# Optimization experiments

Measured on AMD Instinct MI355X. Metric: run time of the kernel, lower is better.

## Reference

```python
import jax, jax.numpy as jnp
import numpy as np

LEAK = 0.01  # PyTorch LeakyReLU default negative_slope


def _leaky(x):
    return jnp.where(x >= 0, x, LEAK * x)


def _sim1(x, ws):
    # 7-layer 1x1-conv MLP applied per pixel; x: (..., Cin, H, W)
    n = len(ws)
    for i, w in enumerate(ws):
        x = jnp.einsum('oc,...chw->...ohw', w, x)
        if i < n - 1:
            x = _leaky(x)
    return x


def setup_inputs() -> dict:
    key = jax.random.key(0)
    ks = jax.random.split(key, 9)
    B, C, S, K = 8, 256, 15, 17
    d = {
        'template_feature': jax.random.normal(ks[0], (B, C, S, S), jnp.float32),
        'candidate_feature': jax.random.normal(ks[1], (B, C, S + K - 1, S + K - 1), jnp.float32),
    }
    chans = [(C, 2 * C), (C // 2, C), (C // 4, C // 2), (C // 8, C // 4),
             (C // 16, C // 8), (C // 32, C // 16), (1, C // 32)]
    for i, (o, c) in enumerate(chans):
        # kaiming_normal_ fan_out for a 1x1 conv: std = sqrt(2/out_channels)
        d[f'w{i}'] = jax.random.normal(ks[2 + i], (o, c), jnp.float32) * np.sqrt(2.0 / o).astype(np.float32)
    return d


def reference(template_feature, candidate_feature, w0, w1, w2, w3, w4, w5, w6):
    ws = (w0, w1, w2, w3, w4, w5, w6)
    B, C, S, _ = template_feature.shape
    K = 17  # sliding-window grid (31-15+1)

    # ---- template branch ----
    t_mean = jnp.mean(template_feature, axis=(-2, -1), keepdims=True)
    rep = jnp.concatenate([jnp.broadcast_to(t_mean, template_feature.shape),
                           template_feature], axis=1)  # (B, 2C, S, S)
    w = _sim1(rep, ws)  # (B, 1, S, S)
    wn = jax.nn.softmax(w.reshape(B, 1, -1), axis=2).reshape(B, 1, S, S)
    common_template = jnp.sum(template_feature * wn, axis=(-2, -1)).reshape(B, C, 1, 1)

    # ---- candidate branch: im2col of 15x15 windows over 31x31 -> 17x17 grid ----
    ii = jnp.arange(S)[:, None] + jnp.arange(K)[None, :]  # (S, K): in-window + window-offset
    # cand_all[b,c,i,j,p,q] = candidate[b,c, i+p, j+q]  -> (B, C, S, S, K, K)
    cand_all = candidate_feature[:, :, ii[:, None, :, None], ii[None, :, None, :]]
    c_mean = jnp.mean(cand_all, axis=(2, 3), keepdims=True)  # divide by S*S as in original
    rep_c = jnp.concatenate([jnp.broadcast_to(c_mean, cand_all.shape), cand_all], axis=1)  # (B, 2C, S, S, K, K)
    rep_c = jnp.transpose(rep_c, (0, 4, 5, 1, 2, 3))  # (B, K, K, 2C, S, S)
    w_c = _sim1(rep_c, ws)  # (B, K, K, 1, S, S)
    wcn = jax.nn.softmax(w_c.reshape(B, K, K, 1, -1), axis=-1).reshape(B, K, K, 1, S, S)
    wcn = jnp.transpose(wcn, (0, 3, 4, 5, 1, 2))  # (B, 1, S, S, K, K)
    common_candidate = jnp.sum(cand_all * wcn, axis=(2, 3))  # (B, C, K, K)

    return common_template, common_candidate
```

## Files before the change

### kernel.cpp

```cpp
#include <hip/hip_runtime.h>

typedef _Float16 half_t;
typedef half_t half4 __attribute__((ext_vector_type(4)));
typedef half_t half8 __attribute__((ext_vector_type(8)));
typedef __fp16 pk16x2 __attribute__((ext_vector_type(2)));
typedef float  f32x4 __attribute__((ext_vector_type(4)));
typedef float  f32x2 __attribute__((ext_vector_type(2)));

static __device__ __forceinline__ half4 pack4(f32x4 a) {
  pk16x2 lo = __builtin_amdgcn_cvt_pkrtz(a[0], a[1]);
  pk16x2 hi = __builtin_amdgcn_cvt_pkrtz(a[2], a[3]);
  half4 h;
  h[0] = lo[0]; h[1] = lo[1]; h[2] = hi[0]; h[3] = hi[1];
  return h;
}

constexpr int B_  = 8;
constexpr int S_  = 15;
constexpr int K_  = 17;
constexpr int P_  = 31;
constexpr int SS_ = 225;
constexpr int PP_ = 961;
constexpr int KK_ = 289;

constexpr int NROW_C = B_ * PP_;
constexpr int NROW_T = B_ * SS_;
constexpr int NROW   = NROW_C + NROW_T;

constexpr int NW0H = 512 * 256;
constexpr int NF16 = 128*256 + 64*128 + 32*64;

constexpr size_t OFF_IN   = 0;
constexpr size_t OFF_OUT0 = OFF_IN   + (size_t)NROW * 256;
constexpr size_t OFF_ROWS = OFF_OUT0 + (size_t)NROW * 512;
constexpr size_t OFF_M0   = OFF_ROWS + (size_t)B_ * 31 * 17 * 256;
constexpr size_t OFF_TM0  = OFF_M0   + (size_t)B_ * KK_ * 256;
constexpr size_t OFF_F16  = OFF_TM0  + (size_t)B_ * 256;

constexpr int X0B  = 0;
constexpr int X1B  = 16384;
constexpr int X3TB = 16384;
constexpr int Y4B  = 25600;
constexpr int SMB  = 32768;
constexpr int REDB = 33728;
constexpr int W4B  = 33792;
constexpr int W5B  = 36096;
constexpr int W6B  = 36736;
constexpr int ROWB = 36768;
constexpr int LDSB = 37248;

__global__ __launch_bounds__(256) void prep_kernel(
    const float* __restrict__ templ, const float* __restrict__ cand,
    const float* __restrict__ w0, const float* __restrict__ w1,
    const float* __restrict__ w2, const float* __restrict__ w3,
    float* __restrict__ inarr, half_t* __restrict__ w0h,
    half_t* __restrict__ w1h, half_t* __restrict__ w2h,
    half_t* __restrict__ w3h)
{
  const int NA = NROW_C * 256;
  const int NB = NROW_T * 256;
  const int total = NA + NB + NW0H + NF16;
  for (int idx = blockIdx.x * blockDim.x + threadIdx.x; idx < total;
       idx += gridDim.x * blockDim.x) {
    if (idx < NA) {
      int c = idx & 255; int r = idx >> 8;
      int q = r % P_; int p = (r / P_) % P_; int b = r / PP_;
      inarr[idx] = cand[((b * 256 + c) * P_ + p) * P_ + q];
    } else if (idx < NA + NB) {
      int t = idx - NA;
      int c = t & 255; int r = t >> 8;
      int j = r % S_; int i = (r / S_) % S_; int b = r / SS_;
      inarr[idx] = templ[((b * 256 + c) * S_ + i) * S_ + j];
    } else if (idx < NA + NB + NW0H) {
      int t = idx - NA - NB;
      int m = t >> 8; int c = t & 255;
      w0h[t] = (half_t)(m < 256 ? w0[m * 512 + 256 + c] : w0[(m - 256) * 512 + c]);
    } else {
      int t = idx - NA - NB - NW0H;
      if (t < 32768)      w1h[t] = (half_t)w1[t];
      else if (t < 40960) w2h[t - 32768] = (half_t)w2[t - 32768];
      else                w3h[t - 40960] = (half_t)w3[t - 40960];
    }
  }
}

__global__ __launch_bounds__(512) void l0gemm_kernel(
    const float* __restrict__ in, const half_t* __restrict__ w0h,
    float* __restrict__ out0)
{
  __shared__ __align__(16) char xls[16 * 512];
  const int tid  = threadIdx.x;
  const int lane = tid & 63;
  const int wvs  = tid >> 6;
  const int row0 = blockIdx.x * 16;

  {
    const int row = tid >> 5;
    const int c8  = (tid & 31) * 8;
    const float* src = in + (size_t)(row0 + row) * 256 + c8;
    half8 h;
#pragma unroll
    for (int r = 0; r < 8; ++r) h[r] = (half_t)src[r];
    const int off = (row * 512 + c8 * 2) ^ ((row & 7) << 4);
    *(half8*)(xls + off) = h;
  }
  __syncthreads();

  const int l15 = lane & 15, g = lane >> 4;
  f32x4 acc[4];
#pragma unroll
  for (int mt = 0; mt < 4; ++mt) acc[mt] = (f32x4){0.f, 0.f, 0.f, 0.f};
#pragma unroll 2
  for (int kb = 0; kb < 8; ++kb) {
    const int off = (l15 * 512 + kb * 64 + g * 16) ^ ((l15 & 7) << 4);
    half8 bfr = *(const half8*)(xls + off);
#pragma unroll
    for (int mt = 0; mt < 4; ++mt) {
      const half_t* ap = w0h + (size_t)((wvs * 4 + mt) * 16 + l15) * 256 + kb * 32 + g * 8;
      half8 a = *(const half8*)ap;
      acc[mt] = __builtin_amdgcn_mfma_f32_16x16x32_f16(a, bfr, acc[mt], 0, 0, 0);
    }
  }
#pragma unroll
  for (int mt = 0; mt < 4; ++mt) {
    const int m0c = (wvs * 4 + mt) * 16 + g * 4;
    *(f32x4*)(out0 + (size_t)(row0 + l15) * 512 + m0c) = acc[mt];
  }
}

__global__ __launch_bounds__(256) void rowsum_kernel(
    const float* __restrict__ out0, float* __restrict__ rows)
{
  const int bid = blockIdx.x;
  const int o = threadIdx.x;
  const int v = bid % 17; const int p = (bid / 17) % 31; const int b = bid / (17 * 31);
  float s = 0.f;
  for (int j = 0; j < 15; ++j)
    s += out0[(size_t)(b * PP_ + p * P_ + v + j) * 512 + 256 + o];
  rows[(size_t)bid * 256 + o] = s;
}

__global__ __launch_bounds__(256) void colsum_kernel(
    const float* __restrict__ rows, float* __restrict__ m0v)
{
  const int bid = blockIdx.x;
  const int o = threadIdx.x;
  const int v = bid % 17; const int u = (bid / 17) % 17; const int b = bid / KK_;
  float s = 0.f;
  for (int i = 0; i < 15; ++i)
    s += rows[(size_t)((b * 31 + u + i) * 17 + v) * 256 + o];
  m0v[(size_t)bid * 256 + o] = s * (1.0f / 225.0f);
}

__global__ __launch_bounds__(256) void tmean0_kernel(
    const float* __restrict__ out0, float* __restrict__ tm0v)
{
  const int b = blockIdx.x;
  const int o = threadIdx.x;
  float s = 0.f;
  for (int t = 0; t < SS_; ++t)
    s += out0[(size_t)(NROW_C + b * SS_ + t) * 512 + 256 + o];
  tm0v[b * 256 + o] = s * (1.0f / 225.0f);
}

__global__ __launch_bounds__(512, 4) void chain_kernel(
    const float* __restrict__ out0, const float* __restrict__ m0v,
    const float* __restrict__ tm0v,
    const half_t* __restrict__ w1h, const half_t* __restrict__ w2h,
    const half_t* __restrict__ w3h,
    const float* __restrict__ w4, const float* __restrict__ w5,
    const float* __restrict__ w6,
    const float* __restrict__ inarr, float* __restrict__ out)
{
  __shared__ __align__(16) char lds[LDSB];
  float*    ldsf   = (float*)lds;
  float*    sm     = (float*)(lds + SMB);
  float*    red    = (float*)(lds + REDB);
  uint16_t* rowoff = (uint16_t*)(lds + ROWB);

  const int tid  = threadIdx.x;
  const int lane = tid & 63;
  const int wvs  = __builtin_amdgcn_readfirstlane(tid >> 6);
  const int bid  = (blockIdx.x & 7) * 290 + (blockIdx.x >> 3);
  const bool is_t = (bid >= B_ * KK_);
  int b, u = 0, v = 0;
  const float* mean_vec;
  if (!is_t) {
    b = bid / KK_;
    int r = bid % KK_;
    u = r / K_; v = r % K_;
    mean_vec = m0v + (size_t)bid * 256;
  } else {
    b = bid - B_ * KK_;
    mean_vec = tm0v + (size_t)b * 256;
  }

  if (tid < SS_) {
    int i = tid / 15, j = tid - i * 15;
    rowoff[tid] = is_t ? (uint16_t)(NROW_C + b * SS_ + tid)
                       : (uint16_t)(b * PP_ + (u + i) * P_ + (v + j));
  }
  ((float*)(lds + W4B))[(tid >> 5) * 36 + (tid & 31)] = w4[tid];
  if (tid < 128) ((float*)(lds + W5B))[(tid >> 4) * 20 + (tid & 15)] = w5[tid];
  if (tid < 8)   ((float*)(lds + W6B))[tid] = w6[tid];

  const half_t* w1base = w1h + (size_t)(16 * wvs + (lane & 15)) * 256 + ((lane >> 4) << 3);
  const int g2 = wvs & 3, h2 = wvs >> 2;
  half8 af2[4];
  {
    const half_t* base = w2h + (size_t)(16 * g2 + (lane & 15)) * 128 + ((lane >> 4) << 3);
#pragma unroll
    for (int kb = 0; kb < 4; ++kb) af2[kb] = *(const half8*)(base + kb * 32);
  }
  const int rt3 = wvs & 1, ct3 = wvs >> 1;
  const half_t* b3ptr = w3h + (size_t)(16 * rt3 + (lane & 15)) * 64 + ((lane >> 4) << 3);
  const int l31 = lane & 31, lhi = lane >> 5;
  const f32x4 mv4a = *(const f32x4*)(mean_vec + 4 * l31);
  const f32x4 mv4b = *(const f32x4*)(mean_vec + 128 + 4 * l31);
  __syncthreads();

  for (int ti = 0; ti < 4; ++ti) {
    const int s0 = ti * 64;
    const int cnt = min(64, SS_ - s0);

    f32x4 acc[4];
#pragma unroll
    for (int nt = 0; nt < 4; ++nt) acc[nt] = (f32x4){0.f, 0.f, 0.f, 0.f};
#pragma unroll
    for (int h = 0; h < 2; ++h) {
      const f32x4 mvh = h ? mv4b : mv4a;
      for (int tt = 0; tt < 4; ++tt) {
        const int pos = 2 * (wvs + tt * 8) + lhi;
        const int srow = rowoff[min(s0 + pos, SS_ - 1)];
        f32x4 x = *(const f32x4*)(out0 + ((size_t)srow << 9) + h * 128 + 4 * l31);
        f32x4 a;
#pragma unroll
        for (int r = 0; r < 4; ++r) {
          float t2 = x[r] + mvh[r];
          a[r] = fmaxf(t2, 0.01f * t2);
        }
        const int off = (pos * 256 + l31 * 8) ^ ((pos & 7) << 4);
        *(half4*)(lds + X0B + off) = pack4(a);
      }
      __syncthreads();

      {
        const half_t* w1p = w1base;
        asm volatile("" : "+v"(w1p));
#pragma unroll 2
        for (int kbp = 0; kbp < 4; ++kbp) {
          half8 a1 = *(const half8*)(w1p + (h * 4 + kbp) * 32);
          const int kbyte = kbp * 64 + ((lane >> 4) << 4);
#pragma unroll
          for (int nt = 0; nt < 4; ++nt) {
            const int pos = nt * 16 + (lane & 15);
            const int off = (pos * 256 + kbyte) ^ ((pos & 7) << 4);
            half8 bfr = *(const half8*)(lds + X0B + off);
            acc[nt] = __builtin_amdgcn_mfma_f32_16x16x32_f16(a1, bfr, acc[nt], 0, 0, 0);
          }
        }
      }
      if (h == 1) {
#pragma unroll
        for (int nt = 0; nt < 4; ++nt) {
          const int pos = nt * 16 + (lane & 15);
          f32x4 a;
#pragma unroll
          for (int r = 0; r < 4; ++r) a[r] = fmaxf(acc[nt][r], 0.01f * acc[nt][r]);
          const int ch0 = 16 * wvs + ((lane >> 4) << 2);
          const int off = (pos * 256 + ch0 * 2) ^ ((pos & 7) << 4);
          *(half4*)(lds + X1B + off) = pack4(a);
        }
      }
      __syncthreads();
    }

    f32x4 acc2[2];
#pragma unroll
    for (int nt = 0; nt < 2; ++nt) acc2[nt] = (f32x4){0.f, 0.f, 0.f, 0.f};
#pragma unroll
    for (int kb = 0; kb < 4; ++kb) {
      const int kbyte = kb * 64 + ((lane >> 4) << 4);
#pragma unroll
      for (int nt = 0; nt < 2; ++nt) {
        const int pos = h2 * 32 + nt * 16 + (lane & 15);
        const int off = (pos * 256 + kbyte) ^ ((pos & 7) << 4);
        half8 bfr = *(const half8*)(lds + X1B + off);
        acc2[nt] = __builtin_amdgcn_mfma_f32_16x16x32_f16(af2[kb], bfr, acc2[nt], 0, 0, 0);
      }
    }
#pragma unroll
    for (int nt = 0; nt < 2; ++nt) {
      const int pos = h2 * 32 + nt * 16 + (lane & 15);
      const int ch0 = 16 * g2 + ((lane >> 4) << 2);
      f32x4 a;
#pragma unroll
      for (int r = 0; r < 4; ++r) a[r] = fmaxf(acc2[nt][r], 0.01f * acc2[nt][r]);
      const int off = (pos * 128 + ch0 * 2) ^ ((pos & 7) << 4);
      *(half4*)(lds + X0B + off) = pack4(a);
    }
    __syncthreads();

    {
      f32x4 acc3 = (f32x4){0.f, 0.f, 0.f, 0.f};
      const int pos = ct3 * 16 + (lane & 15);
#pragma unroll
      for (int kb = 0; kb < 2; ++kb) {
        half8 a3 = *(const half8*)(b3ptr + kb * 32);
        const int kbyte = kb * 64 + ((lane >> 4) << 4);
        const int off = (pos * 128 + kbyte) ^ ((pos & 7) << 4);
        half8 bfr = *(const half8*)(lds + X0B + off);
        acc3 = __builtin_amdgcn_mfma_f32_16x16x32_f16(a3, bfr, acc3, 0, 0, 0);
      }
      const int ch0 = 16 * rt3 + ((lane >> 4) << 2);
      f32x4 o4;
#pragma unroll
      for (int r = 0; r < 4; ++r) o4[r] = fmaxf(acc3[r], 0.01f * acc3[r]);
      *(f32x4*)(lds + X3TB + pos * 144 + ch0 * 4) = o4;
    }
    __syncthreads();

    {
      const int p = lane >> 3, g = lane & 7;
      const int pos = 8 * wvs + p;
      float a4_0 = 0.f, a4_1 = 0.f;
#pragma unroll
      for (int c0 = 0; c0 < 32; c0 += 4) {
        f32x4 x  = *(const f32x4*)(lds + X3TB + pos * 144 + c0 * 4);
        f32x4 wA = *(const f32x4*)(lds + W4B + (2 * g) * 144 + c0 * 4);
        f32x4 wB = *(const f32x4*)(lds + W4B + (2 * g + 1) * 144 + c0 * 4);
#pragma unroll
        for (int r = 0; r < 4; ++r) {
          a4_0 = fmaf(wA[r], x[r], a4_0);
          a4_1 = fmaf(wB[r], x[r], a4_1);
        }
      }
      f32x2 y4v;
      y4v[0] = fmaxf(a4_0, 0.01f * a4_0);
      y4v[1] = fmaxf(a4_1, 0.01f * a4_1);
      *(f32x2*)(lds + Y4B + pos * 80 + g * 8) = y4v;
      float a5 = 0.f;
#pragma unroll
      for (int c0 = 0; c0 < 16; c0 += 4) {
        f32x4 x = *(const f32x4*)(lds + Y4B + pos * 80 + c0 * 4);
        f32x4 w = *(const f32x4*)(lds + W5B + g * 80 + c0 * 4);
#pragma unroll
        for (int r = 0; r < 4; ++r) a5 = fmaf(w[r], x[r], a5);
      }
      a5 = fmaxf(a5, 0.01f * a5);
      float t6 = ((float*)(lds + W6B))[g] * a5;
      t6 += __shfl_xor(t6, 1);
      t6 += __shfl_xor(t6, 2);
      t6 += __shfl_xor(t6, 4);
      if (g == 0 && (8 * wvs + p) < cnt) sm[s0 + pos] = t6;
    }
    __syncthreads();
  }

  float vv = (tid < SS_) ? sm[tid] : -1e30f;
  float m = vv;
#pragma unroll
  for (int off = 32; off >= 1; off >>= 1) m = fmaxf(m, __shfl_xor(m, off));
  if (lane == 0) red[wvs] = m;
  __syncthreads();
  m = red[0];
#pragma unroll
  for (int w = 1; w < 8; ++w) m = fmaxf(m, red[w]);
  float e = (tid < SS_) ? __expf(vv - m) : 0.f;
  float ss = e;
#pragma unroll
  for (int off = 32; off >= 1; off >>= 1) ss += __shfl_xor(ss, off);
  __syncthreads();
  if (lane == 0) red[wvs] = ss;
  __syncthreads();
  float Stot = red[0];
#pragma unroll
  for (int w = 1; w < 8; ++w) Stot += red[w];
  if (tid < SS_) sm[tid] = e / Stot;
  __syncthreads();

  {
    const int c2 = (tid & 127) * 2;
    const int q  = tid >> 7;
    float accx = 0.f, accy = 0.f;
    for (int s = q; s < SS_; s += 4) {
      f32x2 ft = *(const f32x2*)(inarr + ((size_t)rowoff[s] << 8) + c2);
      float w = sm[s];
      accx = fmaf(w, ft[0], accx);
      accy = fmaf(w, ft[1], accy);
    }
    __syncthreads();
    ldsf[q * 256 + c2]     = accx;
    ldsf[q * 256 + c2 + 1] = accy;
    __syncthreads();
    if (tid < 256) {
      float tot = ldsf[tid] + ldsf[256 + tid] + ldsf[512 + tid] + ldsf[768 + tid];
      if (!is_t) out[2048 + ((size_t)(b * 256 + tid) * 17 + u) * 17 + v] = tot;
      else       out[b * 256 + tid] = tot;
    }
  }
}

extern "C" void kernel_launch(void* const* d_in, const int* in_sizes, int n_in,
                              void* d_out, int out_size, void* d_ws, size_t ws_size,
                              hipStream_t stream)
{
  const float* templ = (const float*)d_in[0];
  const float* cand  = (const float*)d_in[1];
  const float* w0 = (const float*)d_in[2];
  const float* w1 = (const float*)d_in[3];
  const float* w2 = (const float*)d_in[4];
  const float* w3 = (const float*)d_in[5];
  const float* w4 = (const float*)d_in[6];
  const float* w5 = (const float*)d_in[7];
  const float* w6 = (const float*)d_in[8];

  float* ws    = (float*)d_ws;
  float* inarr = ws + OFF_IN;
  float* out0  = ws + OFF_OUT0;
  float* rows  = ws + OFF_ROWS;
  float* m0v   = ws + OFF_M0;
  float* tm0v  = ws + OFF_TM0;
  half_t* w0h  = (half_t*)(ws + OFF_F16);
  half_t* w1h  = w0h + NW0H;
  half_t* w2h  = w1h + 128 * 256;
  half_t* w3h  = w2h + 64 * 128;
  float* outf  = (float*)d_out;

  prep_kernel<<<2048, 256, 0, stream>>>(templ, cand, w0, w1, w2, w3,
                                        inarr, w0h, w1h, w2h, w3h);
  l0gemm_kernel<<<NROW / 16, 512, 0, stream>>>(inarr, w0h, out0);
  rowsum_kernel<<<B_ * 31 * 17, 256, 0, stream>>>(out0, rows);
  colsum_kernel<<<B_ * KK_, 256, 0, stream>>>(rows, m0v);
  tmean0_kernel<<<B_, 256, 0, stream>>>(out0, tm0v);
  chain_kernel<<<B_ * KK_ + B_, 512, 0, stream>>>(out0, m0v, tm0v,
                                                  w1h, w2h, w3h, w4, w5, w6,
                                                  inarr, outf);
}
```

Baseline: 302.2 us.

## Transpose input features via LDS tiles and stage full K=256 layer-1 operand

Splits the prep kernel into an LDS-tiled transpose kernel for the input features and a separate weight-conversion kernel. The old transpose read the NCHW input with a stride per thread, so global reads were uncoalesced. In the chain kernel, the layer-1 input is now staged into shared memory as all 256 channels at once, which removes the two-half loop and one barrier per tile. The price is about 16KB more LDS per block, which may lower occupancy, plus one extra kernel launch.

```diff
diff --git a/kernel.cpp b/kernel.cpp
--- a/kernel.cpp
+++ b/kernel.cpp
@@ -38,45 +38,66 @@
 constexpr size_t OFF_F16  = OFF_TM0  + (size_t)B_ * 256;
 
 constexpr int X0B  = 0;
-constexpr int X1B  = 16384;
-constexpr int X3TB = 16384;
-constexpr int Y4B  = 25600;
-constexpr int SMB  = 32768;
-constexpr int REDB = 33728;
-constexpr int W4B  = 33792;
-constexpr int W5B  = 36096;
-constexpr int W6B  = 36736;
-constexpr int ROWB = 36768;
-constexpr int LDSB = 37248;
-
-__global__ __launch_bounds__(256) void prep_kernel(
+constexpr int X1B  = 32768;
+constexpr int X3TB = 32768;
+constexpr int Y4B  = 41984;
+constexpr int SMB  = 49152;
+constexpr int REDB = 50112;
+constexpr int W4B  = 50176;
+constexpr int W5B  = 52480;
+constexpr int W6B  = 53120;
+constexpr int ROWB = 53152;
+constexpr int LDSB = 53632;
+
+__global__ __launch_bounds__(256) void featT_kernel(
     const float* __restrict__ templ, const float* __restrict__ cand,
+    float* __restrict__ inarr)
+{
+  __shared__ float tile[32 * 257];
+  const int bid = blockIdx.x;
+  const float* src;
+  int base, npos, rowbase;
+  if (bid < B_ * 31) {
+    int b = bid / 31, ch = bid % 31;
+    src = cand + (size_t)b * 256 * PP_;
+    base = ch * 32; npos = min(32, PP_ - base);
+    rowbase = b * PP_ + base;
+  } else {
+    int t = bid - B_ * 31;
+    int b = t / 8, ch = t % 8;
+    src = templ + (size_t)b * 256 * SS_;
+    base = ch * 32; npos = min(32, SS_ - base);
+    rowbase = NROW_C + b * SS_ + base;
+  }
+  const int tid = threadIdx.x;
+  const int p  = tid & 31;
+  const int c8 = tid >> 5;
+  const int stride = (bid < B_ * 31) ? PP_ : SS_;
+  if (p < npos) {
+    for (int it = 0; it < 32; ++it) {
+      int c = c8 * 32 + it;
+      tile[p * 257 + c] = src[(size_t)c * stride + base + p];
+    }
+  }
+  __syncthreads();
+  for (int pp = 0; pp < npos; ++pp)
+    inarr[(size_t)(rowbase + pp) * 256 + tid] = tile[pp * 257 + tid];
+}
+
+__global__ __launch_bounds__(256) void wcvt_kernel(
     const float* __restrict__ w0, const float* __restrict__ w1,
     const float* __restrict__ w2, const float* __restrict__ w3,
-    float* __restrict__ inarr, half_t* __restrict__ w0h,
-    half_t* __restrict__ w1h, half_t* __restrict__ w2h,
-    half_t* __restrict__ w3h)
-{
-  const int NA = NROW_C * 256;
-  const int NB = NROW_T * 256;
-  const int total = NA + NB + NW0H + NF16;
+    half_t* __restrict__ w0h, half_t* __restrict__ w1h,
+    half_t* __restrict__ w2h, half_t* __restrict__ w3h)
+{
+  const int total = NW0H + NF16;
   for (int idx = blockIdx.x * blockDim.x + threadIdx.x; idx < total;
        idx += gridDim.x * blockDim.x) {
-    if (idx < NA) {
-      int c = idx & 255; int r = idx >> 8;
-      int q = r % P_; int p = (r / P_) % P_; int b = r / PP_;
-      inarr[idx] = cand[((b * 256 + c) * P_ + p) * P_ + q];
-    } else if (idx < NA + NB) {
-      int t = idx - NA;
-      int c = t & 255; int r = t >> 8;
-      int j = r % S_; int i = (r / S_) % S_; int b = r / SS_;
-      inarr[idx] = templ[((b * 256 + c) * S_ + i) * S_ + j];
-    } else if (idx < NA + NB + NW0H) {
-      int t = idx - NA - NB;
-      int m = t >> 8; int c = t & 255;
-      w0h[t] = (half_t)(m < 256 ? w0[m * 512 + 256 + c] : w0[(m - 256) * 512 + c]);
+    if (idx < NW0H) {
+      int m = idx >> 8; int c = idx & 255;
+      w0h[idx] = (half_t)(m < 256 ? w0[m * 512 + 256 + c] : w0[(m - 256) * 512 + c]);
     } else {
-      int t = idx - NA - NB - NW0H;
+      int t = idx - NW0H;
       if (t < 32768)      w1h[t] = (half_t)w1[t];
       else if (t < 40960) w2h[t - 32768] = (half_t)w2[t - 32768];
       else                w3h[t - 40960] = (half_t)w3[t - 40960];
@@ -214,66 +235,68 @@
   }
   const int rt3 = wvs & 1, ct3 = wvs >> 1;
   const half_t* b3ptr = w3h + (size_t)(16 * rt3 + (lane & 15)) * 64 + ((lane >> 4) << 3);
-  const int l31 = lane & 31, lhi = lane >> 5;
-  const f32x4 mv4a = *(const f32x4*)(mean_vec + 4 * l31);
-  const f32x4 mv4b = *(const f32x4*)(mean_vec + 128 + 4 * l31);
+  const int c8  = (lane & 31) * 8;
+  const int lhi = lane >> 5;
+  const f32x4 mv8a = *(const f32x4*)(mean_vec + c8);
+  const f32x4 mv8b = *(const f32x4*)(mean_vec + c8 + 4);
   __syncthreads();
 
   for (int ti = 0; ti < 4; ++ti) {
     const int s0 = ti * 64;
     const int cnt = min(64, SS_ - s0);
 
+    for (int it = 0; it < 4; ++it) {
+      const int pos = 8 * wvs + it * 2 + lhi;
+      const int srow = rowoff[min(s0 + pos, SS_ - 1)];
+      f32x4 xa = *(const f32x4*)(out0 + ((size_t)srow << 9) + c8);
+      f32x4 xb = *(const f32x4*)(out0 + ((size_t)srow << 9) + c8 + 4);
+      f32x4 a0, a1;
+#pragma unroll
+      for (int r = 0; r < 4; ++r) {
+        float t2 = xa[r] + mv8a[r];
+        a0[r] = fmaxf(t2, 0.01f * t2);
+        float t3 = xb[r] + mv8b[r];
+        a1[r] = fmaxf(t3, 0.01f * t3);
+      }
+      half4 h0 = pack4(a0), h1 = pack4(a1);
+      half8 h8;
+#pragma unroll
+      for (int r = 0; r < 4; ++r) { h8[r] = h0[r]; h8[4 + r] = h1[r]; }
+      const int off = (pos * 512 + c8 * 2) ^ ((pos & 7) << 4);
+      *(half8*)(lds + X0B + off) = h8;
+    }
+    __syncthreads();
+
     f32x4 acc[4];
 #pragma unroll
     for (int nt = 0; nt < 4; ++nt) acc[nt] = (f32x4){0.f, 0.f, 0.f, 0.f};
-#pragma unroll
-    for (int h = 0; h < 2; ++h) {
-      const f32x4 mvh = h ? mv4b : mv4a;
-      for (int tt = 0; tt < 4; ++tt) {
-        const int pos = 2 * (wvs + tt * 8) + lhi;
-        const int srow = rowoff[min(s0 + pos, SS_ - 1)];
-        f32x4 x = *(const f32x4*)(out0 + ((size_t)srow << 9) + h * 128 + 4 * l31);
-        f32x4 a;
-#pragma unroll
-        for (int r = 0; r < 4; ++r) {
-          float t2 = x[r] + mvh[r];
-          a[r] = fmaxf(t2, 0.01f * t2);
-        }
-        const int off = (pos * 256 + l31 * 8) ^ ((pos & 7) << 4);
-        *(half4*)(lds + X0B + off) = pack4(a);
-      }
-      __syncthreads();
-
-      {
-        const half_t* w1p = w1base;
-        asm volatile("" : "+v"(w1p));
+    {
+      const half_t* w1p = w1base;
+      asm volatile("" : "+v"(w1p));
 #pragma unroll 2
-        for (int kbp = 0; kbp < 4; ++kbp) {
-          half8 a1 = *(const half8*)(w1p + (h * 4 + kbp) * 32);
-          const int kbyte = kbp * 64 + ((lane >> 4) << 4);
-#pragma unroll
-          for (int nt = 0; nt < 4; ++nt) {
-            const int pos = nt * 16 + (lane & 15);
-            const int off = (pos * 256 + kbyte) ^ ((pos & 7) << 4);
-            half8 bfr = *(const half8*)(lds + X0B + off);
-            acc[nt] = __builtin_amdgcn_mfma_f32_16x16x32_f16(a1, bfr, acc[nt], 0, 0, 0);
-          }
-        }
-      }
-      if (h == 1) {
+      for (int kb = 0; kb < 8; ++kb) {
+        half8 a1 = *(const half8*)(w1p + kb * 32);
+        const int kbyte = kb * 64 + ((lane >> 4) << 4);
 #pragma unroll
         for (int nt = 0; nt < 4; ++nt) {
           const int pos = nt * 16 + (lane & 15);
-          f32x4 a;
-#pragma unroll
-          for (int r = 0; r < 4; ++r) a[r] = fmaxf(acc[nt][r], 0.01f * acc[nt][r]);
-          const int ch0 = 16 * wvs + ((lane >> 4) << 2);
-          const int off = (pos * 256 + ch0 * 2) ^ ((pos & 7) << 4);
-          *(half4*)(lds + X1B + off) = pack4(a);
+          const int off = (pos * 512 + kbyte) ^ ((pos & 7) << 4);
+          half8 bfr = *(const half8*)(lds + X0B + off);
+          acc[nt] = __builtin_amdgcn_mfma_f32_16x16x32_f16(a1, bfr, acc[nt], 0, 0, 0);
         }
       }
-      __syncthreads();
-    }
+#pragma unroll
+      for (int nt = 0; nt < 4; ++nt) {
+        const int pos = nt * 16 + (lane & 15);
+        f32x4 a;
+#pragma unroll
+        for (int r = 0; r < 4; ++r) a[r] = fmaxf(acc[nt][r], 0.01f * acc[nt][r]);
+        const int ch0 = 16 * wvs + ((lane >> 4) << 2);
+        const int off = (pos * 256 + ch0 * 2) ^ ((pos & 7) << 4);
+        *(half4*)(lds + X1B + off) = pack4(a);
+      }
+    }
+    __syncthreads();
 
     f32x4 acc2[2];
 #pragma unroll
@@ -427,8 +450,8 @@
   half_t* w3h  = w2h + 64 * 128;
   float* outf  = (float*)d_out;
 
-  prep_kernel<<<2048, 256, 0, stream>>>(templ, cand, w0, w1, w2, w3,
-                                        inarr, w0h, w1h, w2h, w3h);
+  featT_kernel<<<B_ * 31 + B_ * 8, 256, 0, stream>>>(templ, cand, inarr);
+  wcvt_kernel<<<256, 256, 0, stream>>>(w0, w1, w2, w3, w0h, w1h, w2h, w3h);
   l0gemm_kernel<<<NROW / 16, 512, 0, stream>>>(inarr, w0h, out0);
   rowsum_kernel<<<B_ * 31 * 17, 256, 0, stream>>>(out0, rows);
   colsum_kernel<<<B_ * KK_, 256, 0, stream>>>(rows, m0v);
```

Result: faster. 277.0 us (-8.3%).
